# Kernel optimization log

Measured on AMD Instinct MI355X. Metric: run time of the kernel, lower is better.

## Reference

```python
import jax, jax.numpy as jnp
from jax import lax
import numpy as np

B, C, H, W = 2, 128, 64, 64
E = 3            # num_experts
DSTATE = 64      # d_state
DCONV = 4        # d_conv
DIN = 2 * C      # d_inner (expand=2)
DTR = 8          # dt_rank = ceil(C/16)
CONVDIM = 64     # router hidden channels


def mamba_block(xseq, in_w, conv_w, conv_b, xproj_w, dt_w, dt_b, A_log, D, out_w):
    # xseq: (B, L, C)
    Bn, L, _ = xseq.shape
    xr = xseq @ in_w.T                      # (B, L, 2*DIN)
    x, res = jnp.split(xr, 2, axis=-1)
    # depthwise causal conv over sequence dim
    xt = x.transpose(0, 2, 1)               # (B, DIN, L)
    xt = lax.conv_general_dilated(xt, conv_w, window_strides=(1,),
                                  padding=[(DCONV - 1, 0)],
                                  feature_group_count=DIN,
                                  dimension_numbers=('NCW', 'OIW', 'NCW'))
    xt = xt + conv_b[None, :, None]
    x = jax.nn.silu(xt.transpose(0, 2, 1))  # (B, L, DIN)
    # input-dependent SSM params
    dbl = x @ xproj_w.T                     # (B, L, DTR + 2*DSTATE)
    dt, Bm, Cm = dbl[..., :DTR], dbl[..., DTR:DTR + DSTATE], dbl[..., DTR + DSTATE:]
    delta = jax.nn.softplus(dt @ dt_w.T + dt_b)  # (B, L, DIN)
    A = -jnp.exp(A_log)                     # (DIN, DSTATE)

    def step(h, inp):
        d_t, B_t, C_t, u_t = inp            # (B,DIN),(B,DSTATE),(B,DSTATE),(B,DIN)
        dA = jnp.exp(d_t[..., None] * A)    # (B, DIN, DSTATE)
        h = dA * h + (d_t * u_t)[..., None] * B_t[:, None, :]
        y = jnp.einsum('bdn,bn->bd', h, C_t)
        return h, y

    h0 = jnp.zeros((Bn, DIN, DSTATE), x.dtype)
    xs = (delta.transpose(1, 0, 2), Bm.transpose(1, 0, 2),
          Cm.transpose(1, 0, 2), x.transpose(1, 0, 2))
    _, ys = lax.scan(step, h0, xs)          # ys: (L, B, DIN)
    y = ys.transpose(1, 0, 2) + x * D       # skip connection
    y = y * jax.nn.silu(res)                # gate
    return y @ out_w.T                      # (B, L, C)


def setup_inputs() -> dict:
    key = jax.random.key(0)
    ks = jax.random.split(key, 10)
    s = 0.02
    n = lambda k, sh: jax.random.normal(k, sh, jnp.float32) * s
    A_log = jnp.log(jnp.broadcast_to(jnp.arange(1, DSTATE + 1, dtype=jnp.float32),
                                     (E, DIN, DSTATE))) + 0.0
    return {
        'x': jax.random.normal(ks[0], (B, C, H, W), jnp.float32),
        'expert_in_w': n(ks[1], (E, 2 * DIN, C)),
        'expert_conv_w': n(ks[2], (E, DIN, 1, DCONV)),
        'expert_conv_b': jnp.zeros((E, DIN), jnp.float32),
        'expert_xproj_w': n(ks[3], (E, DTR + 2 * DSTATE, DIN)),
        'expert_dt_w': n(ks[4], (E, DIN, DTR)),
        'expert_dt_b': jnp.zeros((E, DIN), jnp.float32),
        'expert_A_log': A_log,
        'expert_D': jnp.ones((E, DIN), jnp.float32),
        'expert_out_w': n(ks[5], (E, C, DIN)),
        'router_conv_w': n(ks[6], (CONVDIM, C, 3, 3)),
        'router_conv_b': jnp.zeros((CONVDIM,), jnp.float32),
        'router_lin_w': n(ks[7], (E, CONVDIM)),
        'router_lin_b': jnp.zeros((E,), jnp.float32),
        'fusion_w': n(ks[8], (C, C)),
        'fusion_b': jnp.zeros((C,), jnp.float32),
    }


def reference(x, expert_in_w, expert_conv_w, expert_conv_b, expert_xproj_w,
              expert_dt_w, expert_dt_b, expert_A_log, expert_D, expert_out_w,
              router_conv_w, router_conv_b, router_lin_w, router_lin_b,
              fusion_w, fusion_b):
    Bn, Cn, Hn, Wn = x.shape
    xseq = x.reshape(Bn, Cn, Hn * Wn).transpose(0, 2, 1)  # (B, L, C)
    # router: conv3x3 -> relu -> global avg pool -> linear -> softmax
    r = lax.conv_general_dilated(x, router_conv_w, (1, 1), 'SAME',
                                 dimension_numbers=('NCHW', 'OIHW', 'NCHW'))
    r = jax.nn.relu(r + router_conv_b[None, :, None, None])
    pooled = r.mean(axis=(2, 3))                          # (B, CONVDIM)
    weights = jax.nn.softmax(pooled @ router_lin_w.T + router_lin_b, axis=1)  # (B, E)
    # run all experts via vmap over the expert axis
    outs = jax.vmap(mamba_block, in_axes=(None, 0, 0, 0, 0, 0, 0, 0, 0, 0))(
        xseq, expert_in_w, expert_conv_w, expert_conv_b, expert_xproj_w,
        expert_dt_w, expert_dt_b, expert_A_log, expert_D, expert_out_w)  # (E,B,L,C)
    outs = outs.transpose(0, 1, 3, 2).reshape(outs.shape[0], Bn, Cn, Hn, Wn)
    ws = jnp.einsum('ebchw,be->bchw', outs, weights)
    out = jnp.einsum('bchw,oc->bohw', ws, fusion_w) + fusion_b[None, :, None, None]
    return out
```

## Files before the change

kernel.cpp:

```cpp
#include <hip/hip_runtime.h>
#include <math.h>
#include <stdint.h>

#define LSEQ 4096
#define NCHUNK 8
#define TC 512

#define AS1 __attribute__((address_space(1)))
#define AS3 __attribute__((address_space(3)))
__device__ __forceinline__ void gload_lds16(const void* g, void* l) {
  __builtin_amdgcn_global_load_lds((const AS1 unsigned int*)g,
                                   (AS3 unsigned int*)l, 16, 0, 0);
}

__global__ __launch_bounds__(256) void k_router_conv(
    const float* __restrict__ x, const float* __restrict__ rcw,
    const float* __restrict__ rcb, float* __restrict__ rpool) {
  int bid = blockIdx.x;
  int ocq = bid & 3;
  int h = (bid >> 2) & 63;
  int b = bid >> 8;
  __shared__ float xs[16][3][66];
  __shared__ float wl[16][145];
  int tid = threadIdx.x;
  int ocl = tid & 15;
  int oc = ocq * 16 + ocl;
  int w0 = (tid >> 4) * 4;
  if (tid < 96) {
    int ic = tid / 6, rr = tid % 6;
    int row = rr >> 1, edge = (rr & 1) ? 65 : 0;
    xs[ic][row][edge] = 0.f;
  }
  float acc[4] = {};
  for (int cc = 0; cc < 8; ++cc) {
    __syncthreads();
#pragma unroll
    for (int i = 0; i < 12; ++i) {
      int f = tid + i * 256;
      int ic = f / 192, rem = f % 192;
      int row = rem / 64, w = rem & 63;
      int hh = h - 1 + row;
      float v = 0.f;
      if (hh >= 0 && hh < 64)
        v = x[((size_t)(b * 128 + cc * 16 + ic) * 64 + hh) * 64 + w];
      xs[ic][row][w + 1] = v;
    }
    for (int f = tid; f < 2304; f += 256) {
      int o = f / 144, r = f % 144;
      wl[o][r] = rcw[(size_t)(ocq * 16 + o) * 1152 + cc * 144 + r];
    }
    __syncthreads();
    for (int ic = 0; ic < 16; ++ic) {
#pragma unroll
      for (int kh = 0; kh < 3; ++kh) {
        float xv[6];
#pragma unroll
        for (int j = 0; j < 6; ++j) xv[j] = xs[ic][kh][w0 + j];
        float w_0 = wl[ocl][ic * 9 + kh * 3 + 0];
        float w_1 = wl[ocl][ic * 9 + kh * 3 + 1];
        float w_2 = wl[ocl][ic * 9 + kh * 3 + 2];
#pragma unroll
        for (int i = 0; i < 4; ++i)
          acc[i] += w_0 * xv[i] + w_1 * xv[i + 1] + w_2 * xv[i + 2];
      }
    }
  }
  float cbv = rcb[oc];
  float t = 0.f;
#pragma unroll
  for (int i = 0; i < 4; ++i) t += fmaxf(acc[i] + cbv, 0.f);
  t += __shfl_xor(t, 16);
  t += __shfl_xor(t, 32);
  if ((tid & 63) < 16) atomicAdd(rpool + b * 64 + oc, t);
}

__global__ __launch_bounds__(64) void k_router_softmax(
    const float* __restrict__ rpool, const float* __restrict__ rlw,
    const float* __restrict__ rlb, float* __restrict__ rw) {
  int t = threadIdx.x;
  __shared__ float logits[2][3];
  for (int b = 0; b < 2; ++b) {
    float p = rpool[b * 64 + t] * (1.0f / 4096.0f);
    for (int e = 0; e < 3; ++e) {
      float v = p * rlw[e * 64 + t];
      for (int off = 32; off; off >>= 1) v += __shfl_xor(v, off);
      if (t == 0) logits[b][e] = v + rlb[e];
    }
  }
  __syncthreads();
  if (t == 0) {
    for (int b = 0; b < 2; ++b) {
      float m = fmaxf(fmaxf(logits[b][0], logits[b][1]), logits[b][2]);
      float e0 = expf(logits[b][0] - m), e1 = expf(logits[b][1] - m),
            e2 = expf(logits[b][2] - m);
      float s = e0 + e1 + e2;
      rw[b * 3 + 0] = e0 / s;
      rw[b * 3 + 1] = e1 / s;
      rw[b * 3 + 2] = e2 / s;
    }
  }
}

__global__ __launch_bounds__(256) void k_wfuse(
    const float* __restrict__ fw, const float* __restrict__ outw,
    float* __restrict__ wf) {
  int e = blockIdx.x >> 7;
  int co = blockIdx.x & 127;
  int k = threadIdx.x;
  float acc = 0.f;
  const float* fwr = fw + (size_t)co * 128;
  const float* ob = outw + (size_t)e * 128 * 256 + k;
#pragma unroll 8
  for (int m = 0; m < 128; ++m) acc = fmaf(fwr[m], ob[(size_t)m * 256], acc);
  wf[((size_t)e * 128 + co) * 256 + k] = acc;
}

__global__ __launch_bounds__(256) void k_gemm_in(
    const float* __restrict__ x, const float* __restrict__ inw,
    float* __restrict__ xr) {
  int eb = blockIdx.y;
  int e = eb >> 1, b = eb & 1;
  int lt = blockIdx.x >> 3;
  int jt = blockIdx.x & 7;
  int l0 = lt * 128, j0 = jt * 64;
  __shared__ float xt[16][128];
  __shared__ float wt[16][64];
  int tid = threadIdx.x;
  int jj = (tid & 15) * 4;
  int lr = (tid >> 4) * 8;
  float acc[8][4] = {};
  const float* xb = x + (size_t)b * 128 * 4096;
  const float* wb = inw + (size_t)e * 512 * 128;
  for (int c0 = 0; c0 < 128; c0 += 16) {
    __syncthreads();
#pragma unroll
    for (int i = 0; i < 2; ++i) {
      int f = tid + i * 256;
      int c = f >> 5;
      int lp = (f & 31) * 4;
      float4 v = *(const float4*)(xb + (size_t)(c0 + c) * 4096 + l0 + lp);
      *(float4*)(&xt[c][lp]) = v;
    }
    {
      int j = tid >> 2;
      int kk = (tid & 3) * 4;
      float4 v = *(const float4*)(wb + (size_t)(j0 + j) * 128 + c0 + kk);
      wt[kk + 0][j] = v.x; wt[kk + 1][j] = v.y;
      wt[kk + 2][j] = v.z; wt[kk + 3][j] = v.w;
    }
    __syncthreads();
#pragma unroll
    for (int k = 0; k < 16; ++k) {
      float4 bv = *(const float4*)(&wt[k][jj]);
      float4 a0 = *(const float4*)(&xt[k][lr]);
      float4 a1 = *(const float4*)(&xt[k][lr + 4]);
      float av[8] = {a0.x, a0.y, a0.z, a0.w, a1.x, a1.y, a1.z, a1.w};
#pragma unroll
      for (int i = 0; i < 8; ++i) {
        acc[i][0] = fmaf(av[i], bv.x, acc[i][0]);
        acc[i][1] = fmaf(av[i], bv.y, acc[i][1]);
        acc[i][2] = fmaf(av[i], bv.z, acc[i][2]);
        acc[i][3] = fmaf(av[i], bv.w, acc[i][3]);
      }
    }
  }
  float* out = xr + (size_t)eb * 4096 * 512;
#pragma unroll
  for (int i = 0; i < 8; ++i) {
    float4 v = {acc[i][0], acc[i][1], acc[i][2], acc[i][3]};
    *(float4*)(out + (size_t)(l0 + lr + i) * 512 + j0 + jj) = v;
  }
}

__global__ __launch_bounds__(256) void k_conv1d(
    const float* __restrict__ xr, const float* __restrict__ cw,
    const float* __restrict__ cb, float* __restrict__ xact) {
  int eb = blockIdx.y;
  int e = eb >> 1;
  int l0 = blockIdx.x * 64;
  int d = threadIdx.x;
  const float* w = cw + (size_t)(e * 256 + d) * 4;
  float w0_ = w[0], w1_ = w[1], w2_ = w[2], w3_ = w[3];
  float bias = cb[e * 256 + d];
  const float* xin = xr + (size_t)eb * 4096 * 512 + d;
  float* xo = xact + (size_t)eb * 4096 * 256 + d;
  float xm3 = (l0 >= 3) ? xin[(size_t)(l0 - 3) * 512] : 0.f;
  float xm2 = (l0 >= 2) ? xin[(size_t)(l0 - 2) * 512] : 0.f;
  float xm1 = (l0 >= 1) ? xin[(size_t)(l0 - 1) * 512] : 0.f;
  for (int i = 0; i < 64; ++i) {
    float xc = xin[(size_t)(l0 + i) * 512];
    float v = bias + w0_ * xm3 + w1_ * xm2 + w2_ * xm1 + w3_ * xc;
    xo[(size_t)(l0 + i) * 256] = v / (1.0f + expf(-v));
    xm3 = xm2; xm2 = xm1; xm1 = xc;
  }
}

__global__ __launch_bounds__(256) void k_gemm_xproj(
    const float* __restrict__ xact, const float* __restrict__ xpw,
    float* __restrict__ dbl) {
  int eb = blockIdx.y;
  int e = eb >> 1;
  int lt = blockIdx.x / 3, jt = blockIdx.x % 3;
  int l0 = lt * 128, j0 = jt * 64;
  __shared__ float at[16][128];
  __shared__ float wt[16][64];
  int tid = threadIdx.x;
  int jj = (tid & 15) * 4;
  int lr = (tid >> 4) * 8;
  float acc[8][4] = {};
  const float* ab = xact + (size_t)eb * 4096 * 256;
  const float* wb = xpw + (size_t)e * 136 * 256;
  for (int k0 = 0; k0 < 256; k0 += 16) {
    __syncthreads();
#pragma unroll
    for (int i = 0; i < 2; ++i) {
      int f = tid + i * 256;
      int l = f >> 2, kq = (f & 3) * 4;
      float4 v = *(const float4*)(ab + (size_t)(l0 + l) * 256 + k0 + kq);
      at[kq + 0][l] = v.x; at[kq + 1][l] = v.y;
      at[kq + 2][l] = v.z; at[kq + 3][l] = v.w;
    }
    {
      int j = tid >> 2, kk = (tid & 3) * 4;
      float4 v = {0, 0, 0, 0};
      if (j0 + j < 136)
        v = *(const float4*)(wb + (size_t)(j0 + j) * 256 + k0 + kk);
      wt[kk + 0][j] = v.x; wt[kk + 1][j] = v.y;
      wt[kk + 2][j] = v.z; wt[kk + 3][j] = v.w;
    }
    __syncthreads();
#pragma unroll
    for (int k = 0; k < 16; ++k) {
      float4 bv = *(const float4*)(&wt[k][jj]);
      float4 a0 = *(const float4*)(&at[k][lr]);
      float4 a1 = *(const float4*)(&at[k][lr + 4]);
      float av[8] = {a0.x, a0.y, a0.z, a0.w, a1.x, a1.y, a1.z, a1.w};
#pragma unroll
      for (int i = 0; i < 8; ++i) {
        acc[i][0] = fmaf(av[i], bv.x, acc[i][0]);
        acc[i][1] = fmaf(av[i], bv.y, acc[i][1]);
        acc[i][2] = fmaf(av[i], bv.z, acc[i][2]);
        acc[i][3] = fmaf(av[i], bv.w, acc[i][3]);
      }
    }
  }
  float* ob = dbl + (size_t)eb * 4096 * 136;
  for (int i = 0; i < 8; ++i)
    for (int q = 0; q < 4; ++q) {
      int j = j0 + jj + q;
      if (j < 136) ob[(size_t)(l0 + lr + i) * 136 + j] = acc[i][q];
    }
}

__global__ __launch_bounds__(256) void k_delta(
    const float* __restrict__ dbl, const float* __restrict__ dtw,
    const float* __restrict__ dtb, const float* __restrict__ xact,
    float* __restrict__ dd) {
  int eb = blockIdx.y;
  int e = eb >> 1;
  int t0 = blockIdx.x * 64;
  int d = threadIdx.x;
  __shared__ float dt8[64][8];
  {
    int f = threadIdx.x;
    for (int i = 0; i < 2; ++i, f += 256) {
      int l = f >> 3, r = f & 7;
      dt8[l][r] = dbl[(size_t)eb * 4096 * 136 + (size_t)(t0 + l) * 136 + r];
    }
  }
  __syncthreads();
  float w[8];
#pragma unroll
  for (int r = 0; r < 8; ++r) w[r] = dtw[(size_t)(e * 256 + d) * 8 + r];
  float bias = dtb[e * 256 + d];
  const float* xa = xact + (size_t)eb * 4096 * 256 + d;
  float4* out = (float4*)dd + (size_t)(eb * 256 + d) * 2048 + (t0 >> 1);
  for (int i = 0; i < 64; i += 2) {
    float v0 = bias, v1 = bias;
#pragma unroll
    for (int r = 0; r < 8; ++r) {
      v0 += dt8[i][r] * w[r];
      v1 += dt8[i + 1][r] * w[r];
    }
    float de0 = fmaxf(v0, 0.f) + log1pf(expf(-fabsf(v0)));
    float de1 = fmaxf(v1, 0.f) + log1pf(expf(-fabsf(v1)));
    float u0 = xa[(size_t)(t0 + i) * 256];
    float u1 = xa[(size_t)(t0 + i + 1) * 256];
    float4 o = {de0, de0 * u0, de1, de1 * u1};
    out[i >> 1] = o;
  }
}

__global__ __launch_bounds__(256) void k_scan1(
    const float* __restrict__ dbl, const float* __restrict__ dd,
    const float* __restrict__ alog, float* __restrict__ prd,
    float* __restrict__ hend) {
  __shared__ float sB[2][16][64];
  int eb = blockIdx.y;
  int e = eb >> 1;
  int c = blockIdx.x >> 6;
  int dgrp = blockIdx.x & 63;
  int wid = threadIdx.x >> 6, lane = threadIdx.x & 63;
  int d = dgrp * 4 + wid;
  float An2 = -__expf(alog[((size_t)e * 256 + d) * 64 + lane]) * 1.44269504f;
  const float2* ddp = (const float2*)dd + ((size_t)eb * 256 + d) * 4096;
  {
    uint64_t a = (uint64_t)ddp;
    uint32_t lo = __builtin_amdgcn_readfirstlane((int)(uint32_t)a);
    uint32_t hi = __builtin_amdgcn_readfirstlane((int)(uint32_t)(a >> 32));
    ddp = (const float2*)(((uint64_t)hi << 32) | (uint64_t)lo);
  }
  const float* dblb = dbl + (size_t)eb * 4096 * 136;
  int t0 = c * TC;
  int srow = 4 * wid + (lane >> 4);
  int scol = (lane & 15) * 4;
  float h = 0.f, sdel = 0.f;
  gload_lds16(dblb + (size_t)(t0 + srow) * 136 + 8 + scol, &sB[0][4 * wid][0]);
  __syncthreads();
  for (int s = 0; s < 32; ++s) {
    int cur = s & 1;
    int t0s = t0 + s * 16;
    if (s + 1 < 32)
      gload_lds16(dblb + (size_t)(t0s + 16 + srow) * 136 + 8 + scol,
                  &sB[cur ^ 1][4 * wid][0]);
    float2 rdv[16];
#pragma unroll
    for (int j = 0; j < 16; ++j) rdv[j] = ddp[t0s + j];
#pragma unroll
    for (int j = 0; j < 16; ++j) {
      float Bn = sB[cur][j][lane];
      h = fmaf(exp2f(rdv[j].x * An2), h, rdv[j].y * Bn);
      sdel += rdv[j].x;
    }
    __syncthreads();
  }
  size_t o = (((size_t)eb * 256 + d) * NCHUNK + c) * 64 + lane;
  prd[o] = exp2f(An2 * sdel);
  hend[o] = h;
}

__global__ __launch_bounds__(256) void k_scan2(
    const float* __restrict__ prd, const float* __restrict__ hend,
    float* __restrict__ hinit) {
  int w = blockIdx.x * 4 + (threadIdx.x >> 6);
  int lane = threadIdx.x & 63;
  size_t base = (size_t)w * NCHUNK * 64 + lane;
  float h = 0.f;
  hinit[base] = 0.f;
#pragma unroll
  for (int c = 1; c < NCHUNK; ++c) {
    h = fmaf(prd[base + (c - 1) * 64], h, hend[base + (c - 1) * 64]);
    hinit[base + c * 64] = h;
  }
}

__global__ __launch_bounds__(256) void k_scan3(
    const float* __restrict__ dbl, const float* __restrict__ dd,
    const float* __restrict__ alog, const float* __restrict__ hinit,
    float* __restrict__ ytr) {
  __shared__ float sBC[2][8][128];
  __shared__ float P[4][8][65];
  int eb = blockIdx.y;
  int e = eb >> 1;
  int c = blockIdx.x >> 6;
  int dgrp = blockIdx.x & 63;
  int wid = threadIdx.x >> 6, lane = threadIdx.x & 63;
  int d = dgrp * 4 + wid;
  float An2 = -__expf(alog[((size_t)e * 256 + d) * 64 + lane]) * 1.44269504f;
  const float2* ddp = (const float2*)dd + ((size_t)eb * 256 + d) * 4096;
  {
    uint64_t a = (uint64_t)ddp;
    uint32_t lo = __builtin_amdgcn_readfirstlane((int)(uint32_t)a);
    uint32_t hi = __builtin_amdgcn_readfirstlane((int)(uint32_t)(a >> 32));
    ddp = (const float2*)(((uint64_t)hi << 32) | (uint64_t)lo);
  }
  const float* dblb = dbl + (size_t)eb * 4096 * 136;
  int t0 = c * TC;
  int scol = (lane & 31) * 4;
  int srow = 2 * wid + (lane >> 5);
  float h = hinit[(((size_t)eb * 256 + d) * NCHUNK + c) * 64 + lane];
  float* yout = ytr + ((size_t)eb * 256 + d) * 4096;
  int r = lane & 7, q = lane >> 3;
  gload_lds16(dblb + (size_t)(t0 + srow) * 136 + 8 + scol, &sBC[0][2 * wid][0]);
  __syncthreads();
  for (int s = 0; s < 64; ++s) {
    int cur = s & 1;
    int t0s = t0 + s * 8;
    if (s + 1 < 64)
      gload_lds16(dblb + (size_t)(t0s + 8 + srow) * 136 + 8 + scol,
                  &sBC[cur ^ 1][2 * wid][0]);
    float2 rdv[8];
#pragma unroll
    for (int j = 0; j < 8; ++j) rdv[j] = ddp[t0s + j];
#pragma unroll
    for (int j = 0; j < 8; ++j) {
      float Bn = sBC[cur][j][lane];
      float Cn = sBC[cur][j][64 + lane];
      h = fmaf(exp2f(rdv[j].x * An2), h, rdv[j].y * Bn);
      P[wid][j][lane] = h * Cn;
    }
    float acc = 0.f;
#pragma unroll
    for (int k = 0; k < 8; ++k) acc += P[wid][r][q * 8 + k];
    acc += __shfl_xor(acc, 8);
    acc += __shfl_xor(acc, 16);
    acc += __shfl_xor(acc, 32);
    if (lane < 8) yout[t0s + r] = acc;
    __syncthreads();
  }
}

__global__ __launch_bounds__(256) void k_yfuse(
    const float* __restrict__ ytr, const float* __restrict__ xact,
    const float* __restrict__ xr, const float* __restrict__ Dw,
    float* __restrict__ yf) {
  int eb = blockIdx.y;
  int e = eb >> 1;
  int dti = blockIdx.x >> 6, tti = blockIdx.x & 63;
  int d0 = dti * 64, t0 = tti * 64;
  __shared__ float sp[64][65];
  __shared__ float sq[64][65];
  int tid = threadIdx.x;
  int j = tid & 63;
  int r0 = tid >> 6;
  float Dj = Dw[e * 256 + d0 + j];
  const float* xab = xact + (size_t)eb * 4096 * 256;
  const float* xrb = xr + (size_t)eb * 4096 * 512;
#pragma unroll
  for (int it = 0; it < 16; ++it) {
    int r = r0 + it * 4;
    float xa = xab[(size_t)(t0 + r) * 256 + d0 + j];
    float rs = xrb[(size_t)(t0 + r) * 512 + 256 + d0 + j];
    float pch = rs / (1.0f + expf(-rs));
    sp[r][j] = pch;
    sq[r][j] = xa * Dj * pch;
  }
  __syncthreads();
#pragma unroll
  for (int it = 0; it < 16; ++it) {
    int ddr = r0 + it * 4;
    size_t idx = ((size_t)eb * 256 + d0 + ddr) * 4096 + t0 + j;
    float y = ytr[idx];
    yf[idx] = y * sp[j][ddr] + sq[j][ddr];
  }
}

__global__ __launch_bounds__(256) void k_gemm_out2(
    const float* __restrict__ yf, const float* __restrict__ wf,
    const float* __restrict__ rw, const float* __restrict__ fb,
    float* __restrict__ out) {
  int b = blockIdx.y;
  int tt = blockIdx.x >> 1;
  int ct = blockIdx.x & 1;
  int t0 = tt * 64, c0 = ct * 64;
  __shared__ float at[16][66];
  __shared__ float wt[16][64];
  int tid = threadIdx.x;
  int co4 = (tid & 15) * 4;
  int t4 = (tid >> 4) * 4;
  float acc[4][4] = {};
  for (int e = 0; e < 3; ++e) {
    float wbe = rw[b * 3 + e];
    const float* ab = yf + (size_t)(e * 2 + b) * 256 * 4096;
    const float* wb = wf + (size_t)e * 128 * 256;
    for (int k0 = 0; k0 < 256; k0 += 16) {
      __syncthreads();
      {
#pragma unroll
        for (int i = 0; i < 4; ++i) {
          int f = tid + i * 256;
          int t = f & 63, k = f >> 6;
          at[k][t] = ab[(size_t)(k0 + k) * 4096 + t0 + t];
        }
        int jc = tid >> 2, kk = (tid & 3) * 4;
        float4 v = *(const float4*)(wb + (size_t)(c0 + jc) * 256 + k0 + kk);
        wt[kk + 0][jc] = v.x * wbe; wt[kk + 1][jc] = v.y * wbe;
        wt[kk + 2][jc] = v.z * wbe; wt[kk + 3][jc] = v.w * wbe;
      }
      __syncthreads();
#pragma unroll
      for (int k = 0; k < 16; ++k) {
        float4 bv = *(const float4*)(&wt[k][co4]);
        float4 av = *(const float4*)(&at[k][t4]);
        float a_[4] = {av.x, av.y, av.z, av.w};
#pragma unroll
        for (int i = 0; i < 4; ++i) {
          acc[i][0] = fmaf(a_[i], bv.x, acc[i][0]);
          acc[i][1] = fmaf(a_[i], bv.y, acc[i][1]);
          acc[i][2] = fmaf(a_[i], bv.z, acc[i][2]);
          acc[i][3] = fmaf(a_[i], bv.w, acc[i][3]);
        }
      }
    }
  }
#pragma unroll
  for (int o = 0; o < 4; ++o) {
    float bias = fb[c0 + co4 + o];
    float4 v = {acc[0][o] + bias, acc[1][o] + bias, acc[2][o] + bias,
                acc[3][o] + bias};
    *(float4*)(out + ((size_t)(b * 128 + c0 + co4 + o)) * 4096 + t0 + t4) = v;
  }
}

extern "C" void kernel_launch(void* const* d_in, const int* in_sizes, int n_in,
                              void* d_out, int out_size, void* d_ws,
                              size_t ws_size, hipStream_t stream) {
  const float* x    = (const float*)d_in[0];
  const float* inw  = (const float*)d_in[1];
  const float* cw   = (const float*)d_in[2];
  const float* cb   = (const float*)d_in[3];
  const float* xpw  = (const float*)d_in[4];
  const float* dtw  = (const float*)d_in[5];
  const float* dtb  = (const float*)d_in[6];
  const float* alog = (const float*)d_in[7];
  const float* Dw   = (const float*)d_in[8];
  const float* outw = (const float*)d_in[9];
  const float* rcw  = (const float*)d_in[10];
  const float* rcb  = (const float*)d_in[11];
  const float* rlw  = (const float*)d_in[12];
  const float* rlb  = (const float*)d_in[13];
  const float* fw   = (const float*)d_in[14];
  const float* fb   = (const float*)d_in[15];

  float* ws = (float*)d_ws;
  float* XR    = ws;
  float* XACT  = ws + 12582912;
  float* DBL   = ws + 18874368;
  float* DD    = ws + 22216704;
  float* YTR   = ws + 34799616;
  float* MIX   = ws + 41091072;
  float* RPOOL = ws + 42139648;
  float* RW    = ws + 42139776;
  float* YF    = DD;
  float* PRD   = YTR;
  float* HEND  = YTR + 786432;
  float* HINIT = MIX;
  float* WF    = MIX + 786432;

  if (ws_size < (size_t)42139784 * sizeof(float)) return;

  hipMemsetAsync(RPOOL, 0, 128 * sizeof(float), stream);
  k_router_conv<<<512, 256, 0, stream>>>(x, rcw, rcb, RPOOL);
  k_router_softmax<<<1, 64, 0, stream>>>(RPOOL, rlw, rlb, RW);
  k_wfuse<<<384, 256, 0, stream>>>(fw, outw, WF);
  k_gemm_in<<<dim3(256, 6), 256, 0, stream>>>(x, inw, XR);
  k_conv1d<<<dim3(64, 6), 256, 0, stream>>>(XR, cw, cb, XACT);
  k_gemm_xproj<<<dim3(96, 6), 256, 0, stream>>>(XACT, xpw, DBL);
  k_delta<<<dim3(64, 6), 256, 0, stream>>>(DBL, dtw, dtb, XACT, DD);
  k_scan1<<<dim3(64 * 7, 6), 256, 0, stream>>>(DBL, DD, alog, PRD, HEND);
  k_scan2<<<384, 256, 0, stream>>>(PRD, HEND, HINIT);
  k_scan3<<<dim3(64 * NCHUNK, 6), 256, 0, stream>>>(DBL, DD, alog, HINIT, YTR);
  k_yfuse<<<dim3(256, 6), 256, 0, stream>>>(YTR, XACT, XR, Dw, YF);
  k_gemm_out2<<<dim3(128, 2), 256, 0, stream>>>(YF, WF, RW, fb, (float*)d_out);
}
```

Baseline: 609.5 us.

## Transpose B/C tiles in LDS with XOR swizzle and shuffle-reduce scan outputs

```diff
diff --git a/kernel.cpp b/kernel.cpp
--- a/kernel.cpp
+++ b/kernel.cpp
@@ -12,6 +12,11 @@
   __builtin_amdgcn_global_load_lds((const AS1 unsigned int*)g,
                                    (AS3 unsigned int*)l, 16, 0, 0);
 }
+
+#define BT4R(ARR, N, C4) \
+  (*(const float4*)&(ARR)[N][(((C4) ^ ((N)&7)) << 2)])
+#define BT4W(ARR, N, C4) \
+  (*(float4*)&(ARR)[N][(((C4) ^ ((N)&7)) << 2)])
 
 __global__ __launch_bounds__(256) void k_router_conv(
     const float* __restrict__ x, const float* __restrict__ rcw,
@@ -291,11 +296,15 @@
   }
 }
 
-__global__ __launch_bounds__(256) void k_scan1(
+#define S1S(QX, QY, BV)                          \
+  h = fmaf(exp2f((QX)*An2), h, (QY) * (BV));     \
+  sdel += (QX);
+
+__global__ __launch_bounds__(256, 8) void k_scan1(
     const float* __restrict__ dbl, const float* __restrict__ dd,
     const float* __restrict__ alog, float* __restrict__ prd,
     float* __restrict__ hend) {
-  __shared__ float sB[2][16][64];
+  __shared__ float BT[2][64][32];
   int eb = blockIdx.y;
   int e = eb >> 1;
   int c = blockIdx.x >> 6;
@@ -310,27 +319,42 @@
     uint32_t hi = __builtin_amdgcn_readfirstlane((int)(uint32_t)(a >> 32));
     ddp = (const float2*)(((uint64_t)hi << 32) | (uint64_t)lo);
   }
+  const float4* dq = (const float4*)ddp;
   const float* dblb = dbl + (size_t)eb * 4096 * 136;
   int t0 = c * TC;
-  int srow = 4 * wid + (lane >> 4);
-  int scol = (lane & 15) * 4;
+  int qb = t0 >> 1;
   float h = 0.f, sdel = 0.f;
-  gload_lds16(dblb + (size_t)(t0 + srow) * 136 + 8 + scol, &sB[0][4 * wid][0]);
+  float rB[8];
+#pragma unroll
+  for (int k = 0; k < 8; ++k)
+    rB[k] = dblb[(size_t)(t0 + wid * 8 + k) * 136 + 8 + lane];
+  BT4W(BT[0], lane, 2 * wid) = (float4){rB[0], rB[1], rB[2], rB[3]};
+  BT4W(BT[0], lane, 2 * wid + 1) = (float4){rB[4], rB[5], rB[6], rB[7]};
   __syncthreads();
-  for (int s = 0; s < 32; ++s) {
-    int cur = s & 1;
-    int t0s = t0 + s * 16;
-    if (s + 1 < 32)
-      gload_lds16(dblb + (size_t)(t0s + 16 + srow) * 136 + 8 + scol,
-                  &sB[cur ^ 1][4 * wid][0]);
-    float2 rdv[16];
-#pragma unroll
-    for (int j = 0; j < 16; ++j) rdv[j] = ddp[t0s + j];
-#pragma unroll
-    for (int j = 0; j < 16; ++j) {
-      float Bn = sB[cur][j][lane];
-      h = fmaf(exp2f(rdv[j].x * An2), h, rdv[j].y * Bn);
-      sdel += rdv[j].x;
+  for (int i = 0; i < 16; ++i) {
+    int cur = i & 1;
+    int tb = t0 + i * 32;
+    if (i < 15) {
+#pragma unroll
+      for (int k = 0; k < 8; ++k)
+        rB[k] = dblb[(size_t)(tb + 32 + wid * 8 + k) * 136 + 8 + lane];
+    }
+#pragma unroll
+    for (int g = 0; g < 4; ++g) {
+      int qA = qb + i * 16 + g * 4;
+      float4 q0 = dq[qA + 0], q1 = dq[qA + 1], q2 = dq[qA + 2],
+             q3 = dq[qA + 3];
+      float4 b0 = BT4R(BT[cur], lane, 2 * g);
+      float4 b1 = BT4R(BT[cur], lane, 2 * g + 1);
+      S1S(q0.x, q0.y, b0.x) S1S(q0.z, q0.w, b0.y)
+      S1S(q1.x, q1.y, b0.z) S1S(q1.z, q1.w, b0.w)
+      S1S(q2.x, q2.y, b1.x) S1S(q2.z, q2.w, b1.y)
+      S1S(q3.x, q3.y, b1.z) S1S(q3.z, q3.w, b1.w)
+    }
+    if (i < 15) {
+      BT4W(BT[cur ^ 1], lane, 2 * wid) = (float4){rB[0], rB[1], rB[2], rB[3]};
+      BT4W(BT[cur ^ 1], lane, 2 * wid + 1) =
+          (float4){rB[4], rB[5], rB[6], rB[7]};
     }
     __syncthreads();
   }
@@ -354,12 +378,16 @@
   }
 }
 
-__global__ __launch_bounds__(256) void k_scan3(
+#define S3S(QX, QY, BV, CV, J)                   \
+  h = fmaf(exp2f((QX)*An2), h, (QY) * (BV));     \
+  p[J] = h * (CV);
+
+__global__ __launch_bounds__(256, 5) void k_scan3(
     const float* __restrict__ dbl, const float* __restrict__ dd,
     const float* __restrict__ alog, const float* __restrict__ hinit,
     float* __restrict__ ytr) {
-  __shared__ float sBC[2][8][128];
-  __shared__ float P[4][8][65];
+  __shared__ float BT[2][64][32];
+  __shared__ float CT[2][64][32];
   int eb = blockIdx.y;
   int e = eb >> 1;
   int c = blockIdx.x >> 6;
@@ -374,38 +402,83 @@
     uint32_t hi = __builtin_amdgcn_readfirstlane((int)(uint32_t)(a >> 32));
     ddp = (const float2*)(((uint64_t)hi << 32) | (uint64_t)lo);
   }
+  const float4* dq = (const float4*)ddp;
   const float* dblb = dbl + (size_t)eb * 4096 * 136;
   int t0 = c * TC;
-  int scol = (lane & 31) * 4;
-  int srow = 2 * wid + (lane >> 5);
+  int qb = t0 >> 1;
   float h = hinit[(((size_t)eb * 256 + d) * NCHUNK + c) * 64 + lane];
   float* yout = ytr + ((size_t)eb * 256 + d) * 4096;
-  int r = lane & 7, q = lane >> 3;
-  gload_lds16(dblb + (size_t)(t0 + srow) * 136 + 8 + scol, &sBC[0][2 * wid][0]);
+  int toff = ((lane & 1) << 2) | (lane & 2) | ((lane >> 2) & 1);
+  float rB[8], rC[8];
+#pragma unroll
+  for (int k = 0; k < 8; ++k) {
+    size_t row = (size_t)(t0 + wid * 8 + k) * 136;
+    rB[k] = dblb[row + 8 + lane];
+    rC[k] = dblb[row + 72 + lane];
+  }
+  BT4W(BT[0], lane, 2 * wid) = (float4){rB[0], rB[1], rB[2], rB[3]};
+  BT4W(BT[0], lane, 2 * wid + 1) = (float4){rB[4], rB[5], rB[6], rB[7]};
+  BT4W(CT[0], lane, 2 * wid) = (float4){rC[0], rC[1], rC[2], rC[3]};
+  BT4W(CT[0], lane, 2 * wid + 1) = (float4){rC[4], rC[5], rC[6], rC[7]};
   __syncthreads();
-  for (int s = 0; s < 64; ++s) {
-    int cur = s & 1;
-    int t0s = t0 + s * 8;
-    if (s + 1 < 64)
-      gload_lds16(dblb + (size_t)(t0s + 8 + srow) * 136 + 8 + scol,
-                  &sBC[cur ^ 1][2 * wid][0]);
-    float2 rdv[8];
-#pragma unroll
-    for (int j = 0; j < 8; ++j) rdv[j] = ddp[t0s + j];
-#pragma unroll
-    for (int j = 0; j < 8; ++j) {
-      float Bn = sBC[cur][j][lane];
-      float Cn = sBC[cur][j][64 + lane];
-      h = fmaf(exp2f(rdv[j].x * An2), h, rdv[j].y * Bn);
-      P[wid][j][lane] = h * Cn;
-    }
-    float acc = 0.f;
-#pragma unroll
-    for (int k = 0; k < 8; ++k) acc += P[wid][r][q * 8 + k];
-    acc += __shfl_xor(acc, 8);
-    acc += __shfl_xor(acc, 16);
-    acc += __shfl_xor(acc, 32);
-    if (lane < 8) yout[t0s + r] = acc;
+  for (int i = 0; i < 16; ++i) {
+    int cur = i & 1;
+    int tb = t0 + i * 32;
+    if (i < 15) {
+#pragma unroll
+      for (int k = 0; k < 8; ++k) {
+        size_t row = (size_t)(tb + 32 + wid * 8 + k) * 136;
+        rB[k] = dblb[row + 8 + lane];
+        rC[k] = dblb[row + 72 + lane];
+      }
+    }
+#pragma unroll
+    for (int g = 0; g < 4; ++g) {
+      int qA = qb + i * 16 + g * 4;
+      float4 q0 = dq[qA + 0], q1 = dq[qA + 1], q2 = dq[qA + 2],
+             q3 = dq[qA + 3];
+      float4 b0 = BT4R(BT[cur], lane, 2 * g);
+      float4 b1 = BT4R(BT[cur], lane, 2 * g + 1);
+      float4 c0 = BT4R(CT[cur], lane, 2 * g);
+      float4 c1 = BT4R(CT[cur], lane, 2 * g + 1);
+      float p[8];
+      S3S(q0.x, q0.y, b0.x, c0.x, 0) S3S(q0.z, q0.w, b0.y, c0.y, 1)
+      S3S(q1.x, q1.y, b0.z, c0.z, 2) S3S(q1.z, q1.w, b0.w, c0.w, 3)
+      S3S(q2.x, q2.y, b1.x, c1.x, 4) S3S(q2.z, q2.w, b1.y, c1.y, 5)
+      S3S(q3.x, q3.y, b1.z, c1.z, 6) S3S(q3.z, q3.w, b1.w, c1.w, 7)
+      float qq[4];
+      int s0 = lane & 1;
+#pragma unroll
+      for (int j = 0; j < 4; ++j) {
+        float send = s0 ? p[j] : p[j + 4];
+        float keep = s0 ? p[j + 4] : p[j];
+        qq[j] = keep + __shfl_xor(send, 1);
+      }
+      float rr[2];
+      int s1 = (lane >> 1) & 1;
+#pragma unroll
+      for (int j = 0; j < 2; ++j) {
+        float send = s1 ? qq[j] : qq[j + 2];
+        float keep = s1 ? qq[j + 2] : qq[j];
+        rr[j] = keep + __shfl_xor(send, 2);
+      }
+      int s2 = (lane >> 2) & 1;
+      float send = s2 ? rr[0] : rr[1];
+      float keep = s2 ? rr[1] : rr[0];
+      float u = keep + __shfl_xor(send, 4);
+      u += __shfl_xor(u, 8);
+      u += __shfl_xor(u, 16);
+      u += __shfl_xor(u, 32);
+      if (lane < 8) yout[tb + g * 8 + toff] = u;
+    }
+    if (i < 15) {
+      BT4W(BT[cur ^ 1], lane, 2 * wid) = (float4){rB[0], rB[1], rB[2], rB[3]};
+      BT4W(BT[cur ^ 1], lane, 2 * wid + 1) =
+          (float4){rB[4], rB[5], rB[6], rB[7]};
+      BT4W(CT[cur ^ 1], lane, 2 * wid) = (float4){rC[0], rC[1], rC[2], rC[3]};
+      BT4W(CT[cur ^ 1], lane, 2 * wid + 1) =
+          (float4){rC[4], rC[5], rC[6], rC[7]};
+    }
     __syncthreads();
   }
 }
```

New measurement: 621.5 us. Within noise of the previous version (+2.0%).

## Replace LDS-staged scan loads with register double-buffered direct global loads

Applied to the files above, without the earlier changes.

```diff
diff --git a/kernel.cpp b/kernel.cpp
--- a/kernel.cpp
+++ b/kernel.cpp
@@ -6,12 +6,7 @@
 #define NCHUNK 8
 #define TC 512
 
-#define AS1 __attribute__((address_space(1)))
-#define AS3 __attribute__((address_space(3)))
-__device__ __forceinline__ void gload_lds16(const void* g, void* l) {
-  __builtin_amdgcn_global_load_lds((const AS1 unsigned int*)g,
-                                   (AS3 unsigned int*)l, 16, 0, 0);
-}
+#define EXP2R(X) __builtin_amdgcn_exp2f(X)
 
 __global__ __launch_bounds__(256) void k_router_conv(
     const float* __restrict__ x, const float* __restrict__ rcw,
@@ -291,11 +286,19 @@
   }
 }
 
-__global__ __launch_bounds__(256) void k_scan1(
+#define S1R(QX, QY, BV)                          \
+  h = fmaf(EXP2R((QX)*An2), h, (QY) * (BV));     \
+  sdel += (QX);
+#define S1H(R0, R1, R2, R3, BA)                  \
+  S1R(R0.x, R0.y, BA[0]) S1R(R0.z, R0.w, BA[1])  \
+  S1R(R1.x, R1.y, BA[2]) S1R(R1.z, R1.w, BA[3])  \
+  S1R(R2.x, R2.y, BA[4]) S1R(R2.z, R2.w, BA[5])  \
+  S1R(R3.x, R3.y, BA[6]) S1R(R3.z, R3.w, BA[7])
+
+__global__ __launch_bounds__(256, 4) void k_scan1(
     const float* __restrict__ dbl, const float* __restrict__ dd,
     const float* __restrict__ alog, float* __restrict__ prd,
     float* __restrict__ hend) {
-  __shared__ float sB[2][16][64];
   int eb = blockIdx.y;
   int e = eb >> 1;
   int c = blockIdx.x >> 6;
@@ -310,32 +313,34 @@
     uint32_t hi = __builtin_amdgcn_readfirstlane((int)(uint32_t)(a >> 32));
     ddp = (const float2*)(((uint64_t)hi << 32) | (uint64_t)lo);
   }
-  const float* dblb = dbl + (size_t)eb * 4096 * 136;
+  const float4* dq = (const float4*)ddp;
+  const float* gB = dbl + (size_t)eb * 4096 * 136 + 8 + lane;
   int t0 = c * TC;
-  int srow = 4 * wid + (lane >> 4);
-  int scol = (lane & 15) * 4;
+  int qb = t0 >> 1;
   float h = 0.f, sdel = 0.f;
-  gload_lds16(dblb + (size_t)(t0 + srow) * 136 + 8 + scol, &sB[0][4 * wid][0]);
-  __syncthreads();
-  for (int s = 0; s < 32; ++s) {
-    int cur = s & 1;
-    int t0s = t0 + s * 16;
-    if (s + 1 < 32)
-      gload_lds16(dblb + (size_t)(t0s + 16 + srow) * 136 + 8 + scol,
-                  &sB[cur ^ 1][4 * wid][0]);
-    float2 rdv[16];
-#pragma unroll
-    for (int j = 0; j < 16; ++j) rdv[j] = ddp[t0s + j];
-#pragma unroll
-    for (int j = 0; j < 16; ++j) {
-      float Bn = sB[cur][j][lane];
-      h = fmaf(exp2f(rdv[j].x * An2), h, rdv[j].y * Bn);
-      sdel += rdv[j].x;
-    }
-    __syncthreads();
+  float4 ra0 = dq[qb + 0], ra1 = dq[qb + 1], ra2 = dq[qb + 2],
+         ra3 = dq[qb + 3];
+  float Ba[8], Bb[8];
+#pragma unroll
+  for (int j = 0; j < 8; ++j) Ba[j] = gB[(size_t)(t0 + j) * 136];
+  float4 rb0, rb1, rb2, rb3;
+  for (int sb = 0; sb < 32; ++sb) {
+    int tb = t0 + sb * 16;
+    int qA = qb + sb * 8;
+    rb0 = dq[qA + 4]; rb1 = dq[qA + 5]; rb2 = dq[qA + 6]; rb3 = dq[qA + 7];
+#pragma unroll
+    for (int j = 0; j < 8; ++j) Bb[j] = gB[(size_t)(tb + 8 + j) * 136];
+    S1H(ra0, ra1, ra2, ra3, Ba)
+    if (sb + 1 < 32) {
+      ra0 = dq[qA + 8]; ra1 = dq[qA + 9]; ra2 = dq[qA + 10];
+      ra3 = dq[qA + 11];
+#pragma unroll
+      for (int j = 0; j < 8; ++j) Ba[j] = gB[(size_t)(tb + 16 + j) * 136];
+    }
+    S1H(rb0, rb1, rb2, rb3, Bb)
   }
   size_t o = (((size_t)eb * 256 + d) * NCHUNK + c) * 64 + lane;
-  prd[o] = exp2f(An2 * sdel);
+  prd[o] = EXP2R(An2 * sdel);
   hend[o] = h;
 }
 
@@ -354,11 +359,33 @@
   }
 }
 
-__global__ __launch_bounds__(256) void k_scan3(
+#define S3R(QX, QY, BV, CV, JJ)                  \
+  h = fmaf(EXP2R((QX)*An2), h, (QY) * (BV));     \
+  P[wid][JJ][lane] = h * (CV);
+#define S3H(R0, R1, R2, R3, BA, CA, TB)          \
+  S3R(R0.x, R0.y, BA[0], CA[0], 0)               \
+  S3R(R0.z, R0.w, BA[1], CA[1], 1)               \
+  S3R(R1.x, R1.y, BA[2], CA[2], 2)               \
+  S3R(R1.z, R1.w, BA[3], CA[3], 3)               \
+  S3R(R2.x, R2.y, BA[4], CA[4], 4)               \
+  S3R(R2.z, R2.w, BA[5], CA[5], 5)               \
+  S3R(R3.x, R3.y, BA[6], CA[6], 6)               \
+  S3R(R3.z, R3.w, BA[7], CA[7], 7)               \
+  {                                              \
+    float acc_ = 0.f;                            \
+    _Pragma("unroll")                            \
+    for (int k2 = 0; k2 < 8; ++k2)               \
+      acc_ += P[wid][r][q * 8 + k2];             \
+    acc_ += __shfl_xor(acc_, 8);                 \
+    acc_ += __shfl_xor(acc_, 16);                \
+    acc_ += __shfl_xor(acc_, 32);                \
+    if (lane < 8) yout[(TB) + r] = acc_;         \
+  }
+
+__global__ __launch_bounds__(256, 4) void k_scan3(
     const float* __restrict__ dbl, const float* __restrict__ dd,
     const float* __restrict__ alog, const float* __restrict__ hinit,
     float* __restrict__ ytr) {
-  __shared__ float sBC[2][8][128];
   __shared__ float P[4][8][65];
   int eb = blockIdx.y;
   int e = eb >> 1;
@@ -374,39 +401,43 @@
     uint32_t hi = __builtin_amdgcn_readfirstlane((int)(uint32_t)(a >> 32));
     ddp = (const float2*)(((uint64_t)hi << 32) | (uint64_t)lo);
   }
-  const float* dblb = dbl + (size_t)eb * 4096 * 136;
+  const float4* dq = (const float4*)ddp;
+  const float* gB = dbl + (size_t)eb * 4096 * 136 + 8 + lane;
+  const float* gC = gB + 64;
   int t0 = c * TC;
-  int scol = (lane & 31) * 4;
-  int srow = 2 * wid + (lane >> 5);
+  int qb = t0 >> 1;
   float h = hinit[(((size_t)eb * 256 + d) * NCHUNK + c) * 64 + lane];
   float* yout = ytr + ((size_t)eb * 256 + d) * 4096;
   int r = lane & 7, q = lane >> 3;
-  gload_lds16(dblb + (size_t)(t0 + srow) * 136 + 8 + scol, &sBC[0][2 * wid][0]);
-  __syncthreads();
-  for (int s = 0; s < 64; ++s) {
-    int cur = s & 1;
-    int t0s = t0 + s * 8;
-    if (s + 1 < 64)
-      gload_lds16(dblb + (size_t)(t0s + 8 + srow) * 136 + 8 + scol,
-                  &sBC[cur ^ 1][2 * wid][0]);
-    float2 rdv[8];
-#pragma unroll
-    for (int j = 0; j < 8; ++j) rdv[j] = ddp[t0s + j];
+  float4 ra0 = dq[qb + 0], ra1 = dq[qb + 1], ra2 = dq[qb + 2],
+         ra3 = dq[qb + 3];
+  float Ba[8], Bb[8], Ca[8], Cb[8];
+#pragma unroll
+  for (int j = 0; j < 8; ++j) {
+    Ba[j] = gB[(size_t)(t0 + j) * 136];
+    Ca[j] = gC[(size_t)(t0 + j) * 136];
+  }
+  float4 rb0, rb1, rb2, rb3;
+  for (int sb = 0; sb < 32; ++sb) {
+    int tb = t0 + sb * 16;
+    int qA = qb + sb * 8;
+    rb0 = dq[qA + 4]; rb1 = dq[qA + 5]; rb2 = dq[qA + 6]; rb3 = dq[qA + 7];
 #pragma unroll
     for (int j = 0; j < 8; ++j) {
-      float Bn = sBC[cur][j][lane];
-      float Cn = sBC[cur][j][64 + lane];
-      h = fmaf(exp2f(rdv[j].x * An2), h, rdv[j].y * Bn);
-      P[wid][j][lane] = h * Cn;
-    }
-    float acc = 0.f;
-#pragma unroll
-    for (int k = 0; k < 8; ++k) acc += P[wid][r][q * 8 + k];
-    acc += __shfl_xor(acc, 8);
-    acc += __shfl_xor(acc, 16);
-    acc += __shfl_xor(acc, 32);
-    if (lane < 8) yout[t0s + r] = acc;
-    __syncthreads();
+      Bb[j] = gB[(size_t)(tb + 8 + j) * 136];
+      Cb[j] = gC[(size_t)(tb + 8 + j) * 136];
+    }
+    S3H(ra0, ra1, ra2, ra3, Ba, Ca, tb)
+    if (sb + 1 < 32) {
+      ra0 = dq[qA + 8]; ra1 = dq[qA + 9]; ra2 = dq[qA + 10];
+      ra3 = dq[qA + 11];
+#pragma unroll
+      for (int j = 0; j < 8; ++j) {
+        Ba[j] = gB[(size_t)(tb + 16 + j) * 136];
+        Ca[j] = gC[(size_t)(tb + 16 + j) * 136];
+      }
+    }
+    S3H(rb0, rb1, rb2, rb3, Bb, Cb, tb + 8)
   }
 }
 
```

Result: no change. 611.4 us (+0.3%).
